# Kernel tuning notes

Hardware: AMD Instinct MI355X
Metric: run time of the kernel (lower is better)

## Reference

```python
import jax, jax.numpy as jnp
import numpy as np

THEA = 0.5
DELTA = 1.5
IGNORE = 255
K = 19  # num classes (len(weights))
LOSS_WEIGHT = 1.0
MIN_PIXELS = 20.0  # class kept only if pixel count > 20
WEIGHTS = jnp.ones((K,), dtype=jnp.float32)
EPS = 1e-12


def setup_inputs() -> dict:
    key = jax.random.key(0)
    k1, k2 = jax.random.split(key)
    n, c, h, w = 4, 32, 512, 1024
    predict = jax.random.normal(k1, (n, c, h, w), dtype=jnp.float32)
    target = jax.random.randint(k2, (n, h, w), 0, K, dtype=jnp.int32)
    return {"predict": predict, "target": target}


def _loss(predict, target):
    n, c, h, w = predict.shape
    # (n,c,h,w) -> (n*h*w, c), matching predict.permute(0,2,3,1)
    feat = jnp.transpose(predict, (0, 2, 3, 1)).reshape(-1, c)
    seg = target.reshape(-1)
    valid_pix = seg != IGNORE
    seg = jnp.where(valid_pix, seg, K).astype(jnp.int32)  # ignored -> extra segment K
    ones = valid_pix.astype(feat.dtype)

    # per-class counts and means (segment reduce replaces the python class loop)
    counts = jax.ops.segment_sum(ones, seg, num_segments=K + 1)[:K]
    sums = jax.ops.segment_sum(feat * ones[:, None], seg, num_segments=K + 1)[:K]
    centers = sums / jnp.maximum(counts, 1.0)[:, None]  # [K, c]
    valid_cls = counts > MIN_PIXELS
    n_cls = jnp.maximum(jnp.sum(valid_cls.astype(feat.dtype)), 1.0)

    # ---- variance term: relu(||mean - x|| - thea)^2, normalized by #positives ----
    ctr_ext = jnp.concatenate([centers, jnp.zeros((1, c), centers.dtype)], axis=0)
    ctr_pix = ctr_ext[seg]  # gather per-pixel center
    res = jnp.sqrt(jnp.sum((ctr_pix - feat) ** 2, axis=1) + EPS)  # [n*h*w]
    r = jax.nn.relu(res - THEA) * ones
    sq = jax.ops.segment_sum(r * r, seg, num_segments=K + 1)[:K]
    pos = jax.ops.segment_sum((r > 0).astype(feat.dtype), seg, num_segments=K + 1)[:K]
    norml = jnp.maximum(jax.lax.stop_gradient(pos), 1.0)  # numpy count in original: no grad
    loss_var = jnp.sum(jnp.where(valid_cls, WEIGHTS * sq / norml, 0.0)) / n_cls

    # ---- pairwise center distance term ----
    diff = centers[:, None, :] - centers[None, :, :]  # [K, K, c]
    dist = jnp.sqrt(jnp.sum(diff * diff, axis=-1) + EPS)
    pair_mask = valid_cls[:, None] & valid_cls[None, :] & ~jnp.eye(K, dtype=bool)
    d = jax.nn.relu(2.0 * DELTA - dist)
    loss_dis = jnp.sum(jnp.where(pair_mask, d * d, 0.0)) / jnp.maximum(n_cls * (n_cls - 1.0), 1.0)

    # ---- regularization term ----
    loss_reg = jnp.sum(jnp.where(valid_cls, jnp.sqrt(jnp.sum(centers * centers, axis=1) + EPS), 0.0)) / n_cls

    return LOSS_WEIGHT * (loss_var + loss_dis + 0.001 * loss_reg)


def reference(predict, target):
    return _loss(predict, target)
```

## Files before the change

### kernel.cpp

```cpp
#include <hip/hip_runtime.h>


#define K_CLS 19
#define C_CH 32
#define HW_SHIFT 19
#define HW_SIZE (1 << HW_SHIFT)
#define EPSF 1e-12f
#define THEA_F 0.5f
#define TWO_DELTA 3.0f
#define MIN_PIX 20.0f

#define OFF_PSUM 0
#define OFF_PCNT 40960
#define OFF_RED  42240
#define OFF_VRED 42880
#define OFF_VPART 42944
#define WS_FLOATS (OFF_VPART + 2048 * 64)

__device__ __forceinline__ void atomAddF(float* p, float v) {
  unsafeAtomicAdd(p, v);
}

__device__ __forceinline__ float bperm(float v, int byteidx) {
  return __int_as_float(__builtin_amdgcn_ds_bpermute(byteidx, __float_as_int(v)));
}

__global__ __launch_bounds__(256) void k_accum(
    const float* __restrict__ pred, const int* __restrict__ tgt,
    float* __restrict__ ws)
{
  __shared__ float sA[4][K_CLS][64];
  __shared__ float s_w[4][20];
  const int t = threadIdx.x;
  const int w = t >> 6;
  const int lane = t & 63;
  float* colA = &sA[w][0][lane];
#pragma unroll
  for (int k = 0; k < K_CLS; ++k) colA[k << 6] = 0.f;

  if (blockIdx.x < 2048) {
    const int plane = blockIdx.x >> 4;
    const int slab  = blockIdx.x & 15;
    const int n_idx = plane >> 5;
    const int ch    = plane & 31;
    const float* pbase = pred + (((size_t)plane) << HW_SHIFT) + ((size_t)slab << 15);
    const int*   tbase = tgt  + (((size_t)n_idx) << HW_SHIFT) + ((size_t)slab << 15);

    float4 vA = *reinterpret_cast<const float4*>(pbase + t * 4);
    int4   cA = *reinterpret_cast<const int4*>(tbase + t * 4);
#pragma unroll 1
    for (int it = 0; it < 32; ++it) {
      float4 vB; int4 cB;
      if (it + 1 < 32) {
        vB = *reinterpret_cast<const float4*>(pbase + (it + 1) * 1024 + t * 4);
        cB = *reinterpret_cast<const int4*>(tbase + (it + 1) * 1024 + t * 4);
      }
      const float x[4] = {vA.x, vA.y, vA.z, vA.w};
      const int   s[4] = {cA.x, cA.y, cA.z, cA.w};
      const int   k0 = min((unsigned)s[0], 18u), k1 = min((unsigned)s[1], 18u);
      const int   k2 = min((unsigned)s[2], 18u), k3 = min((unsigned)s[3], 18u);
      const float v0 = ((unsigned)s[0] < K_CLS) ? x[0] : 0.f;
      const float v1 = ((unsigned)s[1] < K_CLS) ? x[1] : 0.f;
      const float v2 = ((unsigned)s[2] < K_CLS) ? x[2] : 0.f;
      const float v3 = ((unsigned)s[3] < K_CLS) ? x[3] : 0.f;
      colA[k0 << 6] += v0;
      colA[k1 << 6] += v1;
      colA[k2 << 6] += v2;
      colA[k3 << 6] += v3;
      vA = vB; cA = cB;
    }

    float acc[K_CLS];
#pragma unroll
    for (int k = 0; k < K_CLS; ++k) acc[k] = colA[k << 6];
#pragma unroll
    for (int k = 0; k < K_CLS; ++k) {
      float s = acc[k];
#pragma unroll
      for (int m = 1; m < 64; m <<= 1) s += __shfl_xor(s, m, 64);
      acc[k] = s;
    }
#pragma unroll
    for (int k = 0; k < K_CLS; ++k)
      if (lane == k) s_w[w][k] = acc[k];
    __syncthreads();
    if (t < K_CLS) {
      const int slot = n_idx * 16 + slab;
      ws[OFF_PSUM + ch * (64 * 20) + slot * 20 + t] =
          s_w[0][t] + s_w[1][t] + s_w[2][t] + s_w[3][t];
    }
  } else {
    const int idx = blockIdx.x - 2048;
    const int n_idx = idx >> 4;
    const int slab  = idx & 15;
    const int* tbase = tgt + (((size_t)n_idx) << HW_SHIFT) + ((size_t)slab << 15);

#pragma unroll 1
    for (int it = 0; it < 32; ++it) {
      const int4 c4 = *reinterpret_cast<const int4*>(tbase + it * 1024 + t * 4);
      const int s[4] = {c4.x, c4.y, c4.z, c4.w};
      const int k0 = min((unsigned)s[0], 18u), k1 = min((unsigned)s[1], 18u);
      const int k2 = min((unsigned)s[2], 18u), k3 = min((unsigned)s[3], 18u);
      colA[k0 << 6] += ((unsigned)s[0] < K_CLS) ? 1.f : 0.f;
      colA[k1 << 6] += ((unsigned)s[1] < K_CLS) ? 1.f : 0.f;
      colA[k2 << 6] += ((unsigned)s[2] < K_CLS) ? 1.f : 0.f;
      colA[k3 << 6] += ((unsigned)s[3] < K_CLS) ? 1.f : 0.f;
    }

    float acc[K_CLS];
#pragma unroll
    for (int k = 0; k < K_CLS; ++k) acc[k] = colA[k << 6];
#pragma unroll
    for (int k = 0; k < K_CLS; ++k) {
      float s = acc[k];
#pragma unroll
      for (int m = 1; m < 64; m <<= 1) s += __shfl_xor(s, m, 64);
      acc[k] = s;
    }
#pragma unroll
    for (int k = 0; k < K_CLS; ++k)
      if (lane == k) s_w[w][k] = acc[k];
    __syncthreads();
    if (t < K_CLS) {
      const int slot = n_idx * 16 + slab;
      ws[OFF_PCNT + slot * 20 + t] = s_w[0][t] + s_w[1][t] + s_w[2][t] + s_w[3][t];
    }
  }
}

__global__ __launch_bounds__(64) void k_reduce(float* __restrict__ ws)
{
  const int o = blockIdx.x;
  const int lane = threadIdx.x;
  float a;
  if (o < C_CH * K_CLS) {
    const int ch = o / K_CLS, k = o - ch * K_CLS;
    a = ws[OFF_PSUM + ch * (64 * 20) + lane * 20 + k];
  } else {
    a = ws[OFF_PCNT + lane * 20 + (o - C_CH * K_CLS)];
  }
#pragma unroll
  for (int m = 1; m < 64; m <<= 1) a += __shfl_xor(a, m, 64);
  if (lane == 0) ws[OFF_RED + o] = a;
}

__global__ __launch_bounds__(256) void k_var(
    const float* __restrict__ pred, const int* __restrict__ tgt,
    float* __restrict__ ws)
{
  __shared__ float s_red[640];
  __shared__ float s_w[4][40];
  const int t = threadIdx.x;
  const int w = t >> 6;
  const int lane = t & 63;

  for (int i = t; i < 627; i += 256) s_red[i] = ws[OFF_RED + i];
  __syncthreads();

  const float invc = (lane < K_CLS) ? 1.f / fmaxf(s_red[608 + lane], 1.f) : 0.f;
  float ctrreg[C_CH];
  float c2reg = 0.f;
#pragma unroll
  for (int c = 0; c < C_CH; ++c) {
    ctrreg[c] = (lane < K_CLS) ? s_red[c * K_CLS + lane] * invc : 0.f;
    c2reg = fmaf(ctrreg[c], ctrreg[c], c2reg);
  }

  const size_t px0 = (size_t)blockIdx.x * 1024;
  const int n_idx = (int)(px0 >> HW_SHIFT);
  const int hw = (int)(px0 & (HW_SIZE - 1)) + t * 4;
  const float* pb = pred + (((size_t)(n_idx * C_CH)) << HW_SHIFT) + hw;

  const int4 c4 = *reinterpret_cast<const int4*>(tgt + ((size_t)n_idx << HW_SHIFT) + hw);
  const int cls[4] = {c4.x, c4.y, c4.z, c4.w};
  bool vl[4]; int sc[4]; int idx[4];
#pragma unroll
  for (int j = 0; j < 4; ++j) {
    vl[j] = (unsigned)cls[j] < K_CLS;
    sc[j] = vl[j] ? cls[j] : 0;
    idx[j] = sc[j] << 2;
  }

  float dot[4] = {0.f, 0.f, 0.f, 0.f};
  float nrm[4] = {0.f, 0.f, 0.f, 0.f};
#pragma unroll
  for (int c = 0; c < C_CH; ++c) {
    const float4 x = *reinterpret_cast<const float4*>(pb + ((size_t)c << HW_SHIFT));
    const float cv0 = bperm(ctrreg[c], idx[0]);
    const float cv1 = bperm(ctrreg[c], idx[1]);
    const float cv2 = bperm(ctrreg[c], idx[2]);
    const float cv3 = bperm(ctrreg[c], idx[3]);
    dot[0] = fmaf(x.x, cv0, dot[0]);  nrm[0] = fmaf(x.x, x.x, nrm[0]);
    dot[1] = fmaf(x.y, cv1, dot[1]);  nrm[1] = fmaf(x.y, x.y, nrm[1]);
    dot[2] = fmaf(x.z, cv2, dot[2]);  nrm[2] = fmaf(x.z, x.z, nrm[2]);
    dot[3] = fmaf(x.w, cv3, dot[3]);  nrm[3] = fmaf(x.w, x.w, nrm[3]);
  }

  float acc_sq[K_CLS], acc_pos[K_CLS];
#pragma unroll
  for (int k = 0; k < K_CLS; ++k) { acc_sq[k] = 0.f; acc_pos[k] = 0.f; }
#pragma unroll
  for (int j = 0; j < 4; ++j) {
    const float c2j = bperm(c2reg, idx[j]);
    const float d2 = fmaxf(nrm[j] - 2.f * dot[j] + c2j, 0.f);
    const float r = sqrtf(d2 + EPSF) - THEA_F;
    const bool act = vl[j] && (r > 0.f);
    const float rr = act ? r * r : 0.f;
    const float pp = act ? 1.f : 0.f;
#pragma unroll
    for (int k = 0; k < K_CLS; ++k) {
      const bool b = (sc[j] == k);
      acc_sq[k]  += b ? rr : 0.f;
      acc_pos[k] += b ? pp : 0.f;
    }
  }

#pragma unroll
  for (int k = 0; k < K_CLS; ++k) {
    float a = acc_sq[k], b = acc_pos[k];
#pragma unroll
    for (int m = 1; m < 64; m <<= 1) {
      a += __shfl_xor(a, m, 64);
      b += __shfl_xor(b, m, 64);
    }
    acc_sq[k] = a; acc_pos[k] = b;
  }
#pragma unroll
  for (int k = 0; k < K_CLS; ++k)
    if (lane == k) { s_w[w][k] = acc_sq[k]; s_w[w][20 + k] = acc_pos[k]; }
  __syncthreads();
  if (t < K_CLS) {
    float* vp = ws + OFF_VPART + (size_t)blockIdx.x * 64;
    vp[t]         = s_w[0][t] + s_w[1][t] + s_w[2][t] + s_w[3][t];
    vp[K_CLS + t] = s_w[0][20 + t] + s_w[1][20 + t] + s_w[2][20 + t] + s_w[3][20 + t];
  }
}

__global__ __launch_bounds__(256) void k_vred(float* __restrict__ ws)
{
  const int o = blockIdx.x;
  const int t = threadIdx.x;
  float a = 0.f;
#pragma unroll
  for (int r = 0; r < 8; ++r)
    a += ws[OFF_VPART + (size_t)(t + r * 256) * 64 + o];
#pragma unroll
  for (int m = 1; m < 64; m <<= 1) a += __shfl_xor(a, m, 64);
  __shared__ float s[4];
  if ((t & 63) == 0) s[t >> 6] = a;
  __syncthreads();
  if (t == 0) ws[OFF_VRED + o] = s[0] + s[1] + s[2] + s[3];
}

__global__ __launch_bounds__(1024) void k_final(
    float* __restrict__ ws, float* __restrict__ out)
{
  __shared__ float s_ctr[C_CH * K_CLS];
  __shared__ float s_valid[K_CLS];
  __shared__ float s_red[3];
  __shared__ float s_ncls;
  const int t = threadIdx.x;
  if (t < 3) s_red[t] = 0.f;
  if (t < K_CLS) s_valid[t] = (ws[OFF_RED + C_CH * K_CLS + t] > MIN_PIX) ? 1.f : 0.f;
  for (int i = t; i < C_CH * K_CLS; i += 1024) {
    const int k = i % K_CLS;
    s_ctr[i] = ws[OFF_RED + i] / fmaxf(ws[OFF_RED + C_CH * K_CLS + k], 1.f);
  }
  __syncthreads();

  if (t == 0) {
    float n = 0.f;
    for (int k = 0; k < K_CLS; ++k) n += s_valid[k];
    s_ncls = fmaxf(n, 1.f);
  }
  if (t < K_CLS && s_valid[t] > 0.f) {
    const float sq  = ws[OFF_VRED + t];
    const float pos = ws[OFF_VRED + K_CLS + t];
    atomAddF(&s_red[0], sq / fmaxf(pos, 1.f));
    float nn = 0.f;
#pragma unroll
    for (int ch = 0; ch < C_CH; ++ch) {
      const float cv = s_ctr[ch * K_CLS + t];
      nn = fmaf(cv, cv, nn);
    }
    atomAddF(&s_red[2], sqrtf(nn + EPSF));
  }
  if (t < K_CLS * K_CLS) {
    const int a = t / K_CLS, b = t - (t / K_CLS) * K_CLS;
    if (a != b && s_valid[a] > 0.f && s_valid[b] > 0.f) {
      float dd = 0.f;
#pragma unroll
      for (int ch = 0; ch < C_CH; ++ch) {
        const float df = s_ctr[ch * K_CLS + a] - s_ctr[ch * K_CLS + b];
        dd = fmaf(df, df, dd);
      }
      const float dist = sqrtf(dd + EPSF);
      const float d = fmaxf(TWO_DELTA - dist, 0.f);
      if (d > 0.f) atomAddF(&s_red[1], d * d);
    }
  }
  __syncthreads();
  if (t == 0) {
    const float n = s_ncls;
    out[0] = s_red[0] / n
           + s_red[1] / fmaxf(n * (n - 1.f), 1.f)
           + 0.001f * s_red[2] / n;
  }
}

extern "C" void kernel_launch(void* const* d_in, const int* in_sizes, int n_in,
                              void* d_out, int out_size, void* d_ws, size_t ws_size,
                              hipStream_t stream) {
  const float* pred = (const float*)d_in[0];
  const int*   tgt  = (const int*)d_in[1];
  float* ws  = (float*)d_ws;
  float* out = (float*)d_out;
  const int P = in_sizes[1];
  const int nBlocksVar = P / 1024;

  k_accum <<<2048 + 64, 256, 0, stream>>>(pred, tgt, ws);
  k_reduce<<<C_CH * K_CLS + K_CLS, 64, 0, stream>>>(ws);
  k_var   <<<nBlocksVar, 256, 0, stream>>>(pred, tgt, ws);
  k_vred  <<<2 * K_CLS, 256, 0, stream>>>(ws);
  k_final <<<1, 1024, 0, stream>>>(ws, out);
}
```

Baseline: 441.7 us.

## Pack target labels into bytes for accumulation and double per-thread pixels in variance

```diff
diff --git a/kernel.cpp b/kernel.cpp
--- a/kernel.cpp
+++ b/kernel.cpp
@@ -15,7 +15,8 @@
 #define OFF_RED  42240
 #define OFF_VRED 42880
 #define OFF_VPART 42944
-#define WS_FLOATS (OFF_VPART + 2048 * 64)
+#define OFF_MAP  108480
+#define WS_FLOATS (OFF_MAP + 524288)
 
 __device__ __forceinline__ void atomAddF(float* p, float v) {
   unsafeAtomicAdd(p, v);
@@ -25,15 +26,25 @@
   return __int_as_float(__builtin_amdgcn_ds_bpermute(byteidx, __float_as_int(v)));
 }
 
+__global__ __launch_bounds__(256) void k_pack(
+    const int* __restrict__ tgt, float* __restrict__ ws)
+{
+  const int i = blockIdx.x * 256 + threadIdx.x;
+  const int4 c = *reinterpret_cast<const int4*>(tgt + (size_t)i * 4);
+  const unsigned u = (unsigned)(c.x & 255) | ((unsigned)(c.y & 255) << 8)
+                   | ((unsigned)(c.z & 255) << 16) | ((unsigned)(c.w & 255) << 24);
+  reinterpret_cast<unsigned*>(ws + OFF_MAP)[i] = u;
+}
+
 __global__ __launch_bounds__(256) void k_accum(
-    const float* __restrict__ pred, const int* __restrict__ tgt,
-    float* __restrict__ ws)
+    const float* __restrict__ pred, float* __restrict__ ws)
 {
   __shared__ float sA[4][K_CLS][64];
   __shared__ float s_w[4][20];
   const int t = threadIdx.x;
   const int w = t >> 6;
   const int lane = t & 63;
+  const unsigned* umap = reinterpret_cast<const unsigned*>(ws + OFF_MAP);
   float* colA = &sA[w][0][lane];
 #pragma unroll
   for (int k = 0; k < K_CLS; ++k) colA[k << 6] = 0.f;
@@ -44,30 +55,30 @@
     const int n_idx = plane >> 5;
     const int ch    = plane & 31;
     const float* pbase = pred + (((size_t)plane) << HW_SHIFT) + ((size_t)slab << 15);
-    const int*   tbase = tgt  + (((size_t)n_idx) << HW_SHIFT) + ((size_t)slab << 15);
+    const int mbase = ((n_idx << HW_SHIFT) + (slab << 15)) >> 2;
 
     float4 vA = *reinterpret_cast<const float4*>(pbase + t * 4);
-    int4   cA = *reinterpret_cast<const int4*>(tbase + t * 4);
+    unsigned mA = umap[mbase + t];
 #pragma unroll 1
     for (int it = 0; it < 32; ++it) {
-      float4 vB; int4 cB;
+      float4 vB; unsigned mB;
       if (it + 1 < 32) {
         vB = *reinterpret_cast<const float4*>(pbase + (it + 1) * 1024 + t * 4);
-        cB = *reinterpret_cast<const int4*>(tbase + (it + 1) * 1024 + t * 4);
+        mB = umap[mbase + (it + 1) * 256 + t];
       }
-      const float x[4] = {vA.x, vA.y, vA.z, vA.w};
-      const int   s[4] = {cA.x, cA.y, cA.z, cA.w};
-      const int   k0 = min((unsigned)s[0], 18u), k1 = min((unsigned)s[1], 18u);
-      const int   k2 = min((unsigned)s[2], 18u), k3 = min((unsigned)s[3], 18u);
-      const float v0 = ((unsigned)s[0] < K_CLS) ? x[0] : 0.f;
-      const float v1 = ((unsigned)s[1] < K_CLS) ? x[1] : 0.f;
-      const float v2 = ((unsigned)s[2] < K_CLS) ? x[2] : 0.f;
-      const float v3 = ((unsigned)s[3] < K_CLS) ? x[3] : 0.f;
+      const unsigned b0 = mA & 255u, b1 = (mA >> 8) & 255u;
+      const unsigned b2 = (mA >> 16) & 255u, b3 = mA >> 24;
+      const int   k0 = min(b0, 18u), k1 = min(b1, 18u);
+      const int   k2 = min(b2, 18u), k3 = min(b3, 18u);
+      const float v0 = (b0 < K_CLS) ? vA.x : 0.f;
+      const float v1 = (b1 < K_CLS) ? vA.y : 0.f;
+      const float v2 = (b2 < K_CLS) ? vA.z : 0.f;
+      const float v3 = (b3 < K_CLS) ? vA.w : 0.f;
       colA[k0 << 6] += v0;
       colA[k1 << 6] += v1;
       colA[k2 << 6] += v2;
       colA[k3 << 6] += v3;
-      vA = vB; cA = cB;
+      vA = vB; mA = mB;
     }
 
     float acc[K_CLS];
@@ -91,20 +102,17 @@
     }
   } else {
     const int idx = blockIdx.x - 2048;
-    const int n_idx = idx >> 4;
-    const int slab  = idx & 15;
-    const int* tbase = tgt + (((size_t)n_idx) << HW_SHIFT) + ((size_t)slab << 15);
+    const int mbase = idx << 13;
 
 #pragma unroll 1
     for (int it = 0; it < 32; ++it) {
-      const int4 c4 = *reinterpret_cast<const int4*>(tbase + it * 1024 + t * 4);
-      const int s[4] = {c4.x, c4.y, c4.z, c4.w};
-      const int k0 = min((unsigned)s[0], 18u), k1 = min((unsigned)s[1], 18u);
-      const int k2 = min((unsigned)s[2], 18u), k3 = min((unsigned)s[3], 18u);
-      colA[k0 << 6] += ((unsigned)s[0] < K_CLS) ? 1.f : 0.f;
-      colA[k1 << 6] += ((unsigned)s[1] < K_CLS) ? 1.f : 0.f;
-      colA[k2 << 6] += ((unsigned)s[2] < K_CLS) ? 1.f : 0.f;
-      colA[k3 << 6] += ((unsigned)s[3] < K_CLS) ? 1.f : 0.f;
+      const unsigned m = umap[mbase + it * 256 + t];
+      const unsigned b0 = m & 255u, b1 = (m >> 8) & 255u;
+      const unsigned b2 = (m >> 16) & 255u, b3 = m >> 24;
+      colA[min(b0, 18u) << 6] += (b0 < K_CLS) ? 1.f : 0.f;
+      colA[min(b1, 18u) << 6] += (b1 < K_CLS) ? 1.f : 0.f;
+      colA[min(b2, 18u) << 6] += (b2 < K_CLS) ? 1.f : 0.f;
+      colA[min(b3, 18u) << 6] += (b3 < K_CLS) ? 1.f : 0.f;
     }
 
     float acc[K_CLS];
@@ -122,7 +130,7 @@
       if (lane == k) s_w[w][k] = acc[k];
     __syncthreads();
     if (t < K_CLS) {
-      const int slot = n_idx * 16 + slab;
+      const int slot = idx;
       ws[OFF_PCNT + slot * 20 + t] = s_w[0][t] + s_w[1][t] + s_w[2][t] + s_w[3][t];
     }
   }
@@ -166,50 +174,50 @@
     c2reg = fmaf(ctrreg[c], ctrreg[c], c2reg);
   }
 
-  const size_t px0 = (size_t)blockIdx.x * 1024;
-  const int n_idx = (int)(px0 >> HW_SHIFT);
-  const int hw = (int)(px0 & (HW_SIZE - 1)) + t * 4;
-  const float* pb = pred + (((size_t)(n_idx * C_CH)) << HW_SHIFT) + hw;
-
-  const int4 c4 = *reinterpret_cast<const int4*>(tgt + ((size_t)n_idx << HW_SHIFT) + hw);
-  const int cls[4] = {c4.x, c4.y, c4.z, c4.w};
-  bool vl[4]; int sc[4]; int idx[4];
-#pragma unroll
-  for (int j = 0; j < 4; ++j) {
-    vl[j] = (unsigned)cls[j] < K_CLS;
-    sc[j] = vl[j] ? cls[j] : 0;
-    idx[j] = sc[j] << 2;
-  }
-
-  float dot[4] = {0.f, 0.f, 0.f, 0.f};
-  float nrm[4] = {0.f, 0.f, 0.f, 0.f};
+  const int bpx = blockIdx.x * 2048;
+  const int n_idx = bpx >> HW_SHIFT;
+  const int hw0 = bpx & (HW_SIZE - 1);
+
+  const int* tb = tgt + (((size_t)n_idx) << HW_SHIFT) + hw0;
+  const int4 ca = *reinterpret_cast<const int4*>(tb + t * 4);
+  const int4 cb = *reinterpret_cast<const int4*>(tb + 1024 + t * 4);
+  const int cls[8] = {ca.x, ca.y, ca.z, ca.w, cb.x, cb.y, cb.z, cb.w};
+  int idx8[8];
+#pragma unroll
+  for (int j = 0; j < 8; ++j)
+    idx8[j] = min((unsigned)cls[j], 19u) << 2;
+
+  float nrm[8] = {0.f,0.f,0.f,0.f,0.f,0.f,0.f,0.f};
+  float dot[8] = {0.f,0.f,0.f,0.f,0.f,0.f,0.f,0.f};
 #pragma unroll
   for (int c = 0; c < C_CH; ++c) {
-    const float4 x = *reinterpret_cast<const float4*>(pb + ((size_t)c << HW_SHIFT));
-    const float cv0 = bperm(ctrreg[c], idx[0]);
-    const float cv1 = bperm(ctrreg[c], idx[1]);
-    const float cv2 = bperm(ctrreg[c], idx[2]);
-    const float cv3 = bperm(ctrreg[c], idx[3]);
-    dot[0] = fmaf(x.x, cv0, dot[0]);  nrm[0] = fmaf(x.x, x.x, nrm[0]);
-    dot[1] = fmaf(x.y, cv1, dot[1]);  nrm[1] = fmaf(x.y, x.y, nrm[1]);
-    dot[2] = fmaf(x.z, cv2, dot[2]);  nrm[2] = fmaf(x.z, x.z, nrm[2]);
-    dot[3] = fmaf(x.w, cv3, dot[3]);  nrm[3] = fmaf(x.w, x.w, nrm[3]);
+    const float* cp = pred + (((size_t)(n_idx * C_CH + c)) << HW_SHIFT) + hw0;
+    const float4 xa = *reinterpret_cast<const float4*>(cp + t * 4);
+    const float4 xb = *reinterpret_cast<const float4*>(cp + 1024 + t * 4);
+    const float x[8] = {xa.x, xa.y, xa.z, xa.w, xb.x, xb.y, xb.z, xb.w};
+#pragma unroll
+    for (int j = 0; j < 8; ++j) {
+      const float cv = bperm(ctrreg[c], idx8[j]);
+      nrm[j] = fmaf(x[j], x[j], nrm[j]);
+      dot[j] = fmaf(x[j], cv, dot[j]);
+    }
   }
 
   float acc_sq[K_CLS], acc_pos[K_CLS];
 #pragma unroll
   for (int k = 0; k < K_CLS; ++k) { acc_sq[k] = 0.f; acc_pos[k] = 0.f; }
 #pragma unroll
-  for (int j = 0; j < 4; ++j) {
-    const float c2j = bperm(c2reg, idx[j]);
+  for (int j = 0; j < 8; ++j) {
+    const float c2j = bperm(c2reg, idx8[j]);
     const float d2 = fmaxf(nrm[j] - 2.f * dot[j] + c2j, 0.f);
     const float r = sqrtf(d2 + EPSF) - THEA_F;
-    const bool act = vl[j] && (r > 0.f);
+    const bool act = ((unsigned)cls[j] < K_CLS) && (r > 0.f);
     const float rr = act ? r * r : 0.f;
     const float pp = act ? 1.f : 0.f;
+    const int sc = min((unsigned)cls[j], 18u);
 #pragma unroll
     for (int k = 0; k < K_CLS; ++k) {
-      const bool b = (sc[j] == k);
+      const bool b = (sc == k);
       acc_sq[k]  += b ? rr : 0.f;
       acc_pos[k] += b ? pp : 0.f;
     }
@@ -242,7 +250,7 @@
   const int t = threadIdx.x;
   float a = 0.f;
 #pragma unroll
-  for (int r = 0; r < 8; ++r)
+  for (int r = 0; r < 4; ++r)
     a += ws[OFF_VPART + (size_t)(t + r * 256) * 64 + o];
 #pragma unroll
   for (int m = 1; m < 64; m <<= 1) a += __shfl_xor(a, m, 64);
@@ -316,11 +324,11 @@
   float* ws  = (float*)d_ws;
   float* out = (float*)d_out;
   const int P = in_sizes[1];
-  const int nBlocksVar = P / 1024;
-
-  k_accum <<<2048 + 64, 256, 0, stream>>>(pred, tgt, ws);
+
+  k_pack  <<<P / 1024, 256, 0, stream>>>(tgt, ws);
+  k_accum <<<2048 + 64, 256, 0, stream>>>(pred, ws);
   k_reduce<<<C_CH * K_CLS + K_CLS, 64, 0, stream>>>(ws);
-  k_var   <<<nBlocksVar, 256, 0, stream>>>(pred, tgt, ws);
+  k_var   <<<P / 2048, 256, 0, stream>>>(pred, tgt, ws);
   k_vred  <<<2 * K_CLS, 256, 0, stream>>>(ws);
   k_final <<<1, 1024, 0, stream>>>(ws, out);
 }
```

After: 443.9 us. Within noise of the previous version (+0.5%).
